# Kernel tuning notes

Measured on AMD Instinct MI355X. Metric: run time of the kernel, lower is better.

Reference implementation:

```python
import jax, jax.numpy as jnp
import numpy as np
import math

NUM_SEGS = 16  # label ids in gt are in [0, NUM_SEGS); 0 = background
NP_RATIO = 3
PI = np.float32(math.pi)


def cart2polar(coord):
    # coord: (N, 2, H, W) -> normalized polar angle in [0, 1)
    x = coord[:, 0]
    y = coord[:, 1]
    theta = jnp.arctan(y / (x + np.float32(1e-12)))
    theta = theta + (x < 0).astype(coord.dtype) * PI
    theta = theta + ((x > 0) & (y < 0)).astype(coord.dtype) * (2 * PI)
    return theta / (2 * PI)


def cal_weight(gt2d):
    # gt2d: (H, W) int labels. Per-segment average weight:
    # each pixel of segment s>0 gets (posCount / nSegPresent) / count(s).
    flat = gt2d.reshape(-1)
    counts = jnp.zeros((NUM_SEGS,), jnp.float32).at[flat].add(1.0)
    pos_counts = counts.at[0].set(0.0)  # labels = unique(gt)[1:] drops background 0
    pos_count = pos_counts.sum()
    nseg = (pos_counts > 0).sum().astype(jnp.float32)
    seg_ave = pos_count / jnp.maximum(nseg, 1.0)
    pix = seg_ave / jnp.maximum(counts, 1.0)  # per-label pixel weight
    return jnp.where(gt2d > 0, pix[gt2d], np.float32(0.0))


def setup_inputs() -> dict:
    key = jax.random.key(0)
    k1, k2, k3 = jax.random.split(key, 3)
    N, C, H, W = 8, 2, 1024, 1024
    pred = jax.random.normal(k1, (N, C, H, W), dtype=jnp.float32)
    gt_df = jax.random.normal(k2, (N, C, H, W), dtype=jnp.float32)
    gt = jax.random.randint(k3, (N, 1, H, W), 0, NUM_SEGS, dtype=jnp.int32)
    return {"pred": pred, "gt_df": gt_df, "gt": gt}


def reference(pred, gt_df, gt):
    N, _, H, W = pred.shape
    dist = pred - gt_df
    distL2 = dist * dist
    angle = cart2polar(gt_df) - cart2polar(pred)          # (N,H,W)
    term = distL2[:, 0] + distL2[:, 1] + angle * angle    # (N,H,W)

    weight = jax.vmap(lambda g: cal_weight(g[0]))(gt)     # (N,H,W) positive-region weights
    regionNeg = (weight == 0).astype(jnp.float32)
    sumPos = (weight > 0).astype(jnp.float32).sum(axis=(1, 2))
    sumNeg = regionNeg.sum(axis=(1, 2))
    k = jnp.minimum(NP_RATIO * sumPos, sumNeg).astype(jnp.int32)  # hard negatives per sample

    # OHEM: keep the k largest negative-region losses per sample
    lossFlat = (term * regionNeg).reshape(N, H * W)
    order = jnp.argsort(lossFlat, axis=1)
    rank = jnp.argsort(order, axis=1)  # rank of each element in ascending order
    keep = rank >= (H * W - k[:, None])
    mask = (keep & (lossFlat != 0)).astype(jnp.float32).reshape(N, H, W)  # weightNeg indicator

    # Faithful to torch broadcast: weightPos (N,H,W) + weightNeg (N,1,H,W) -> (N,N,H,W),
    # computed here without materializing the (N,N,H,W) tensor:
    # sum_{i,j,hw} term[j]*(weight[j] + mask[i]) = N*sum(term*weight) + sum_hw(term.sum(0)*mask.sum(0))
    num = N * jnp.sum(term * weight) + jnp.sum(term.sum(axis=0) * mask.sum(axis=0))
    denom = N * (weight.sum() + mask.sum())
    return num / N / 2.0 / denom
```

## Files before the change

kernel.cpp:

```cpp
#include <hip/hip_runtime.h>
#include <math.h>

#define NBATCH 8
#define HWN (1024*1024)
#define NGRP (HWN/4)
#define NSEG 16
#define N2B 512


static __device__ __forceinline__ float polar01(float x, float y) {
    float r = y * __builtin_amdgcn_rcpf(x + 1e-12f);
    float ar = fabsf(r);
    float inv = __builtin_amdgcn_rcpf(ar);
    bool big = ar > 1.0f;
    float t = big ? inv : ar;
    float s = t * t;
    float p = -0.0117212f;
    p = fmaf(p, s,  0.05265332f);
    p = fmaf(p, s, -0.11643287f);
    p = fmaf(p, s,  0.19354346f);
    p = fmaf(p, s, -0.33262348f);
    p = fmaf(p, s,  0.99997726f);
    float a = t * p;
    a = big ? (1.57079632679489662f - a) : a;
    a = copysignf(a, r);
    if (x < 0.f) a += 3.14159274101257324f;
    else if (x > 0.f && y < 0.f) a += 6.28318548202514648f;
    return a * 0.15915494309189535f;
}

static __device__ __forceinline__ void block_reduce2(double& a, double& b) {
    for (int o = 32; o; o >>= 1) { a += __shfl_down(a, o); b += __shfl_down(b, o); }
    __shared__ double sa[4], sb[4];
    int wave = threadIdx.x >> 6, lane = threadIdx.x & 63;
    if (lane == 0) { sa[wave] = a; sb[wave] = b; }
    __syncthreads();
    if (threadIdx.x == 0) {
        a = sa[0] + sa[1] + sa[2] + sa[3];
        b = sb[0] + sb[1] + sb[2] + sb[3];
    }
    __syncthreads();
}

__global__ __launch_bounds__(256) void k_fused(const float* __restrict__ pred,
        const float* __restrict__ gdf, const int* __restrict__ gt,
        float* __restrict__ lossBuf, unsigned short* __restrict__ tsumBuf,
        unsigned* __restrict__ h1G, unsigned* __restrict__ segCG,
        float* __restrict__ segSG) {
    __shared__ unsigned h1[NBATCH * 256];
    __shared__ unsigned sC[4][NBATCH * NSEG];
    __shared__ float    sS[4][NBATCH * NSEG];
    int tid = threadIdx.x, wave = tid >> 6;
    for (int i = tid; i < NBATCH * 256; i += 256) h1[i] = 0u;
    if (tid < NBATCH * NSEG) {
#pragma unroll
        for (int w = 0; w < 4; ++w) { sC[w][tid] = 0u; sS[w][tid] = 0.f; }
    }
    __syncthreads();

    int j = blockIdx.x * 256 + tid;
    float4 tsum = make_float4(0.f, 0.f, 0.f, 0.f);
#pragma unroll 2
    for (int n = 0; n < NBATCH; ++n) {
        float4 px4 = ((const float4*)(pred + ((size_t)(2 * n)    ) * HWN))[j];
        float4 py4 = ((const float4*)(pred + ((size_t)(2 * n) + 1) * HWN))[j];
        float4 gx4 = ((const float4*)(gdf  + ((size_t)(2 * n)    ) * HWN))[j];
        float4 gy4 = ((const float4*)(gdf  + ((size_t)(2 * n) + 1) * HWN))[j];
        int4   g4  = ((const int4*)  (gt   + (size_t)n * HWN))[j];
        float4 lossv;
#pragma unroll
        for (int e = 0; e < 4; ++e) {
            float px = (&px4.x)[e], py = (&py4.x)[e];
            float gx = (&gx4.x)[e], gy = (&gy4.x)[e];
            int   g  = (&g4.x)[e] & 15;
            float dx = px - gx, dy = py - gy;
            float ang = polar01(gx, gy) - polar01(px, py);
            float t = dx * dx + dy * dy + ang * ang;
            (&tsum.x)[e] += t;
            atomicAdd(&sC[wave][n * NSEG + g], 1u);
            atomicAdd(&sS[wave][n * NSEG + g], t);
            float lv = (g == 0) ? t : 0.f;
            (&lossv.x)[e] = lv;
            unsigned u = __float_as_uint(lv);
            if (u) atomicAdd(&h1[n * 256 + (u >> 24)], 1u);
        }
        ((float4*)(lossBuf + (size_t)n * HWN))[j] = lossv;
    }
    ushort4 tz;
#pragma unroll
    for (int e = 0; e < 4; ++e) {
        unsigned u = __float_as_uint((&tsum.x)[e]);
        (&tz.x)[e] = (unsigned short)((u + 0x7FFFu + ((u >> 16) & 1u)) >> 16);
    }
    ((ushort4*)tsumBuf)[j] = tz;

    __syncthreads();
    int copy = blockIdx.x & 31;
    if (tid < NBATCH * NSEG) {
        unsigned c = sC[0][tid] + sC[1][tid] + sC[2][tid] + sC[3][tid];
        float    s = sS[0][tid] + sS[1][tid] + sS[2][tid] + sS[3][tid];
        atomicAdd(&segCG[copy * (NBATCH * NSEG) + tid], c);
        atomicAdd(&segSG[copy * (NBATCH * NSEG) + tid], s);
    }
    for (int i = tid; i < NBATCH * 256; i += 256) {
        unsigned v = h1[i];
        if (v) atomicAdd(&h1G[copy * 2048 + i], v);
    }
}

__global__ void k_scanA(const unsigned* __restrict__ h1G, const unsigned* __restrict__ segCG,
                        const float* __restrict__ segSG, unsigned* __restrict__ stMode,
                        unsigned* __restrict__ stPfx, unsigned* __restrict__ stK,
                        unsigned* __restrict__ stT, double* __restrict__ num1w) {
    int n = blockIdx.x, tid = threadIdx.x;
    __shared__ unsigned h[256];
    __shared__ unsigned cc[NSEG];
    __shared__ double   sd[NSEG];
    unsigned hv = 0;
    for (int c = 0; c < 32; ++c) hv += h1G[c * 2048 + n * 256 + tid];
    h[tid] = hv;
    if (tid < NSEG) {
        unsigned cv = 0; double sv = 0.0;
        for (int c = 0; c < 32; ++c) {
            cv += segCG[c * (NBATCH * NSEG) + n * NSEG + tid];
            sv += (double)segSG[c * (NBATCH * NSEG) + n * NSEG + tid];
        }
        cc[tid] = cv; sd[tid] = sv;
    }
    __syncthreads();
    if (tid == 0) {
        long long sumPos = 0; int nseg = 0;
        for (int s = 1; s < NSEG; ++s) { sumPos += cc[s]; nseg += cc[s] ? 1 : 0; }
        long long sumNeg = cc[0];
        float seg_ave = (float)sumPos / (float)(nseg ? nseg : 1);
        double num1 = 0.0, wsum = 0.0;
        for (int s = 1; s < NSEG; ++s) {
            float pix = seg_ave / (float)(cc[s] ? cc[s] : 1u);
            num1 += (double)pix * sd[s];
            wsum += (double)pix * (double)cc[s];
        }
        num1w[2 * n] = num1; num1w[2 * n + 1] = wsum;
        long long k = 3 * sumPos; if (sumNeg < k) k = sumNeg;
        unsigned nnz = 0;
        for (int b = 0; b < 256; ++b) nnz += h[b];
        if (k <= 0)                      { stMode[n] = 0u; stT[n] = 0xFFFFFFFFu; stPfx[n] = 0u; stK[n] = 0u; }
        else if (k >= (long long)nnz)    { stMode[n] = 0u; stT[n] = 0u;          stPfx[n] = 0u; stK[n] = 0u; }
        else {
            unsigned cum = 0; int b1 = 0;
            for (int b = 255; b >= 0; --b) { if (cum + h[b] >= (unsigned)k) { b1 = b; break; } cum += h[b]; }
            stMode[n] = 1u; stPfx[n] = (unsigned)b1; stK[n] = (unsigned)k - cum; stT[n] = 0u;
        }
    }
}

__global__ __launch_bounds__(256) void k_refine(const float* __restrict__ lossBuf,
        const unsigned* __restrict__ stMode, const unsigned* __restrict__ stPfx,
        unsigned* __restrict__ hist, int level) {
    unsigned md[NBATCH], pf[NBATCH]; bool any = false;
#pragma unroll
    for (int n = 0; n < NBATCH; ++n) {
        md[n] = stMode[n]; pf[n] = stPfx[n];
        any = any || (md[n] == (unsigned)level);
    }
    if (!any) return;
    int ms = 32 - 8 * level, hs = 24 - 8 * level;
    int stride = gridDim.x * blockDim.x;
    for (int j = blockIdx.x * blockDim.x + threadIdx.x; j < NGRP; j += stride) {
#pragma unroll
        for (int n = 0; n < NBATCH; ++n) {
            if (md[n] != (unsigned)level) continue;
            float4 lv = ((const float4*)(lossBuf + (size_t)n * HWN))[j];
#pragma unroll
            for (int e = 0; e < 4; ++e) {
                unsigned u = __float_as_uint((&lv.x)[e]);
                if (u != 0u && (u >> ms) == pf[n])
                    atomicAdd(&hist[n * 256 + ((u >> hs) & 255u)], 1u);
            }
        }
    }
}

__global__ void k_scanN(unsigned* __restrict__ stMode, unsigned* __restrict__ stPfx,
                        unsigned* __restrict__ stK, unsigned* __restrict__ stT,
                        const unsigned* __restrict__ hist, int level) {
    int n = blockIdx.x;
    if (stMode[n] != (unsigned)level) return;
    __shared__ unsigned h[256];
    h[threadIdx.x] = hist[n * 256 + threadIdx.x];
    __syncthreads();
    if (threadIdx.x == 0) {
        unsigned k2 = stK[n], cum = 0; int bb = 0;
        for (int b = 255; b >= 0; --b) { if (cum + h[b] >= k2) { bb = b; break; } cum += h[b]; }
        unsigned np = (stPfx[n] << 8) | (unsigned)bb;
        stK[n] = k2 - cum;
        if (level == 3) { stT[n] = np; stMode[n] = 0u; }
        else            { stPfx[n] = np; stMode[n] = (unsigned)(level + 1); }
    }
}

__global__ __launch_bounds__(256) void k_num2(const float* __restrict__ lossBuf,
        const unsigned short* __restrict__ tsumBuf, const unsigned* __restrict__ stT,
        double* __restrict__ partB) {
    unsigned T[NBATCH];
#pragma unroll
    for (int n = 0; n < NBATCH; ++n) T[n] = stT[n];
    double acc = 0.0, cnt = 0.0;
    int stride = gridDim.x * blockDim.x;
    for (int j = blockIdx.x * blockDim.x + threadIdx.x; j < NGRP; j += stride) {
        ushort4 tz = ((const ushort4*)tsumBuf)[j];
        float ts[4];
#pragma unroll
        for (int e = 0; e < 4; ++e) ts[e] = __uint_as_float(((unsigned)(&tz.x)[e]) << 16);
#pragma unroll
        for (int n = 0; n < NBATCH; ++n) {
            float4 lv = ((const float4*)(lossBuf + (size_t)n * HWN))[j];
#pragma unroll
            for (int e = 0; e < 4; ++e) {
                unsigned u = __float_as_uint((&lv.x)[e]);
                if (u != 0u && u >= T[n]) { acc += (double)ts[e]; cnt += 1.0; }
            }
        }
    }
    block_reduce2(acc, cnt);
    if (threadIdx.x == 0) { partB[blockIdx.x * 2] = acc; partB[blockIdx.x * 2 + 1] = cnt; }
}

__global__ void k_result(const double* __restrict__ num1w, const double* __restrict__ partB,
                         float* __restrict__ out) {
    double c = 0.0, d = 0.0;
    for (int i = threadIdx.x; i < N2B; i += 256) { c += partB[2 * i]; d += partB[2 * i + 1]; }
    block_reduce2(c, d);
    if (threadIdx.x == 0) {
        double num1 = 0.0, wsum = 0.0;
        for (int n = 0; n < NBATCH; ++n) { num1 += num1w[2 * n]; wsum += num1w[2 * n + 1]; }
        double num = (double)NBATCH * num1 + c;
        double denom = (double)NBATCH * (wsum + d);
        out[0] = (float)(num / (double)NBATCH / 2.0 / denom);
    }
}


extern "C" void kernel_launch(void* const* d_in, const int* in_sizes, int n_in,
                              void* d_out, int out_size, void* d_ws, size_t ws_size,
                              hipStream_t stream) {
    const float* pred = (const float*)d_in[0];
    const float* gdf  = (const float*)d_in[1];
    const int*   gt   = (const int*)d_in[2];
    float* out = (float*)d_out;

    char* W = (char*)d_ws;
    float* lossBuf = (float*)W;
    unsigned short* tsumBuf = (unsigned short*)(W + 33554432);
    char* Z = W + 33554432 + 2097152;
    unsigned* h1G   = (unsigned*)Z;
    unsigned* segCG = (unsigned*)(Z + 262144);
    float*    segSG = (float*)  (Z + 262144 + 16384);
    unsigned* hA    = (unsigned*)(Z + 262144 + 32768);
    unsigned* hB    = hA + 2048;
    unsigned* hC    = hB + 2048;
    const size_t ZBYTES = 262144 + 32768 + 3 * 8192;
    char* P = Z + ZBYTES;
    unsigned* stMode = (unsigned*)P;
    unsigned* stPfx  = stMode + 8;
    unsigned* stK    = stMode + 16;
    unsigned* stT    = stMode + 24;
    double* num1w    = (double*)(P + 128);
    double* partB    = (double*)(P + 256);

    size_t need = 33554432 + 2097152 + ZBYTES + 256 + (size_t)N2B * 2 * 8;
    if (ws_size < need) return;

    hipMemsetAsync(Z, 0, ZBYTES, stream);
    k_fused <<<dim3(NGRP / 256), 256, 0, stream>>>(pred, gdf, gt, lossBuf, tsumBuf, h1G, segCG, segSG);
    k_scanA <<<NBATCH, 256, 0, stream>>>(h1G, segCG, segSG, stMode, stPfx, stK, stT, num1w);
    k_refine<<<256, 256, 0, stream>>>(lossBuf, stMode, stPfx, hA, 1);
    k_scanN <<<NBATCH, 256, 0, stream>>>(stMode, stPfx, stK, stT, hA, 1);
    k_refine<<<256, 256, 0, stream>>>(lossBuf, stMode, stPfx, hB, 2);
    k_scanN <<<NBATCH, 256, 0, stream>>>(stMode, stPfx, stK, stT, hB, 2);
    k_refine<<<256, 256, 0, stream>>>(lossBuf, stMode, stPfx, hC, 3);
    k_scanN <<<NBATCH, 256, 0, stream>>>(stMode, stPfx, stK, stT, hC, 3);
    k_num2  <<<N2B, 256, 0, stream>>>(lossBuf, tsumBuf, stT, partB);
    k_result<<<1, 256, 0, stream>>>(num1w, partB, out);
}
```

Measured before the change: 212.4 us.

## Precompute segment weights and skip OHEM selection when all negatives are kept

```diff
diff --git a/kernel.cpp b/kernel.cpp
--- a/kernel.cpp
+++ b/kernel.cpp
@@ -4,8 +4,7 @@
 #define NBATCH 8
 #define HWN (1024*1024)
 #define NGRP (HWN/4)
-#define NSEG 16
-#define N2B 512
+#define MAINB 1024
 
 
 static __device__ __forceinline__ float polar01(float x, float y) {
@@ -32,34 +31,111 @@
 static __device__ __forceinline__ void block_reduce2(double& a, double& b) {
     for (int o = 32; o; o >>= 1) { a += __shfl_down(a, o); b += __shfl_down(b, o); }
     __shared__ double sa[4], sb[4];
-    int wave = threadIdx.x >> 6, lane = threadIdx.x & 63;
-    if (lane == 0) { sa[wave] = a; sb[wave] = b; }
+    int w = threadIdx.x >> 6, l = threadIdx.x & 63;
+    if (l == 0) { sa[w] = a; sb[w] = b; }
+    __syncthreads();
+    if (threadIdx.x == 0) { a = sa[0]+sa[1]+sa[2]+sa[3]; b = sb[0]+sb[1]+sb[2]+sb[3]; }
+    __syncthreads();
+}
+
+static __device__ __forceinline__ void block_reduce3(double& a, double& b, double& c) {
+    for (int o = 32; o; o >>= 1) { a += __shfl_down(a, o); b += __shfl_down(b, o); c += __shfl_down(c, o); }
+    __shared__ double sa[4], sb[4], sc[4];
+    int w = threadIdx.x >> 6, l = threadIdx.x & 63;
+    if (l == 0) { sa[w] = a; sb[w] = b; sc[w] = c; }
     __syncthreads();
     if (threadIdx.x == 0) {
-        a = sa[0] + sa[1] + sa[2] + sa[3];
-        b = sb[0] + sb[1] + sb[2] + sb[3];
-    }
-    __syncthreads();
-}
-
-__global__ __launch_bounds__(256) void k_fused(const float* __restrict__ pred,
+        a = sa[0]+sa[1]+sa[2]+sa[3]; b = sb[0]+sb[1]+sb[2]+sb[3]; c = sc[0]+sc[1]+sc[2]+sc[3];
+    }
+    __syncthreads();
+}
+
+__global__ __launch_bounds__(256) void k_hist(const int* __restrict__ gt,
+        unsigned* __restrict__ countsRep) {
+    int tid = threadIdx.x;
+    int n = blockIdx.x >> 8;
+    int jb = blockIdx.x & 255;
+    const int4* g4 = (const int4*)(gt + (size_t)n * HWN);
+    unsigned c[16];
+#pragma unroll
+    for (int b = 0; b < 16; ++b) c[b] = 0u;
+#pragma unroll
+    for (int k = 0; k < 4; ++k) {
+        int4 g = g4[jb * 1024 + k * 256 + tid];
+#pragma unroll
+        for (int e = 0; e < 4; ++e) {
+            int gv = (&g.x)[e] & 15;
+#pragma unroll
+            for (int b = 0; b < 16; ++b) c[b] += (unsigned)__popcll(__ballot(gv == b));
+        }
+    }
+    if ((tid & 63) == 0) {
+        int copy = (blockIdx.x * 4 + (tid >> 6)) & 31;
+        unsigned* dst = countsRep + copy * 128 + n * 16;
+#pragma unroll
+        for (int b = 0; b < 16; ++b) atomicAdd(&dst[b], c[b]);
+    }
+}
+
+__global__ void k_stats(const unsigned* __restrict__ countsRep, float* __restrict__ pix,
+                        int* __restrict__ kv, int* __restrict__ mode,
+                        double* __restrict__ g_wsum, unsigned* __restrict__ anySlow) {
+    int tid = threadIdx.x;
+    __shared__ unsigned sc[128];
+    __shared__ int smd[NBATCH];
+    __shared__ double sws[NBATCH];
+    if (tid < 128) {
+        unsigned s = 0;
+        for (int c = 0; c < 32; ++c) s += countsRep[c * 128 + tid];
+        sc[tid] = s;
+    }
+    __syncthreads();
+    if (tid < NBATCH) {
+        int n = tid;
+        long long sumPos = 0; int nseg = 0;
+        for (int s = 1; s < 16; ++s) { sumPos += sc[n*16+s]; nseg += sc[n*16+s] ? 1 : 0; }
+        long long sumNeg = sc[n*16];
+        float seg_ave = (float)sumPos / (float)(nseg ? nseg : 1);
+        double ws = 0.0;
+        pix[n*16] = 0.f;
+        for (int s = 1; s < 16; ++s) {
+            unsigned cc = sc[n*16+s];
+            float pv = seg_ave / (float)(cc > 1u ? cc : 1u);
+            pix[n*16+s] = pv;
+            ws += (double)pv * (double)cc;
+        }
+        long long k = 3 * sumPos; if (sumNeg < k) k = sumNeg;
+        kv[n] = (int)k;
+        int md = (k <= 0) ? 0 : ((k >= sumNeg) ? 1 : 2);
+        mode[n] = md; smd[n] = md; sws[n] = ws;
+    }
+    __syncthreads();
+    if (tid == 0) {
+        double w = 0.0; unsigned as = 0u;
+        for (int i = 0; i < NBATCH; ++i) { w += sws[i]; as |= (smd[i] == 2) ? 1u : 0u; }
+        *g_wsum = w; *anySlow = as;
+    }
+}
+
+__global__ __launch_bounds__(256) void k_main(const float* __restrict__ pred,
         const float* __restrict__ gdf, const int* __restrict__ gt,
+        const float* __restrict__ pix, const int* __restrict__ mode,
         float* __restrict__ lossBuf, unsigned short* __restrict__ tsumBuf,
-        unsigned* __restrict__ h1G, unsigned* __restrict__ segCG,
-        float* __restrict__ segSG) {
+        unsigned* __restrict__ h1G, double* __restrict__ pN1,
+        double* __restrict__ pS2, double* __restrict__ pC) {
+    __shared__ float spix[128];
+    __shared__ int smode[NBATCH];
     __shared__ unsigned h1[NBATCH * 256];
-    __shared__ unsigned sC[4][NBATCH * NSEG];
-    __shared__ float    sS[4][NBATCH * NSEG];
-    int tid = threadIdx.x, wave = tid >> 6;
+    int tid = threadIdx.x;
+    if (tid < 128) spix[tid] = pix[tid];
+    if (tid < NBATCH) smode[tid] = mode[tid];
     for (int i = tid; i < NBATCH * 256; i += 256) h1[i] = 0u;
-    if (tid < NBATCH * NSEG) {
-#pragma unroll
-        for (int w = 0; w < 4; ++w) { sC[w][tid] = 0u; sS[w][tid] = 0.f; }
-    }
     __syncthreads();
 
     int j = blockIdx.x * 256 + tid;
-    float4 tsum = make_float4(0.f, 0.f, 0.f, 0.f);
+    float tsum[4] = {0.f, 0.f, 0.f, 0.f};
+    int   cntE[4] = {0, 0, 0, 0};
+    float num1f = 0.f;
 #pragma unroll 2
     for (int n = 0; n < NBATCH; ++n) {
         float4 px4 = ((const float4*)(pred + ((size_t)(2 * n)    ) * HWN))[j];
@@ -67,6 +143,7 @@
         float4 gx4 = ((const float4*)(gdf  + ((size_t)(2 * n)    ) * HWN))[j];
         float4 gy4 = ((const float4*)(gdf  + ((size_t)(2 * n) + 1) * HWN))[j];
         int4   g4  = ((const int4*)  (gt   + (size_t)n * HWN))[j];
+        int m = smode[n];
         float4 lossv;
 #pragma unroll
         for (int e = 0; e < 4; ++e) {
@@ -76,93 +153,88 @@
             float dx = px - gx, dy = py - gy;
             float ang = polar01(gx, gy) - polar01(px, py);
             float t = dx * dx + dy * dy + ang * ang;
-            (&tsum.x)[e] += t;
-            atomicAdd(&sC[wave][n * NSEG + g], 1u);
-            atomicAdd(&sS[wave][n * NSEG + g], t);
-            float lv = (g == 0) ? t : 0.f;
-            (&lossv.x)[e] = lv;
-            unsigned u = __float_as_uint(lv);
-            if (u) atomicAdd(&h1[n * 256 + (u >> 24)], 1u);
-        }
-        ((float4*)(lossBuf + (size_t)n * HWN))[j] = lossv;
+            tsum[e] += t;
+            num1f += t * spix[n * 16 + g];
+            if (m == 1) {
+                if (g == 0 && t != 0.f) cntE[e]++;
+            } else if (m == 2) {
+                float lv = (g == 0) ? t : 0.f;
+                (&lossv.x)[e] = lv;
+                unsigned u = __float_as_uint(lv);
+                if (u) atomicAdd(&h1[n * 256 + (u >> 24)], 1u);
+            }
+        }
+        if (m == 2) ((float4*)(lossBuf + (size_t)n * HWN))[j] = lossv;
     }
     ushort4 tz;
 #pragma unroll
     for (int e = 0; e < 4; ++e) {
-        unsigned u = __float_as_uint((&tsum.x)[e]);
+        unsigned u = __float_as_uint(tsum[e]);
         (&tz.x)[e] = (unsigned short)((u + 0x7FFFu + ((u >> 16) & 1u)) >> 16);
     }
     ((ushort4*)tsumBuf)[j] = tz;
 
-    __syncthreads();
-    int copy = blockIdx.x & 31;
-    if (tid < NBATCH * NSEG) {
-        unsigned c = sC[0][tid] + sC[1][tid] + sC[2][tid] + sC[3][tid];
-        float    s = sS[0][tid] + sS[1][tid] + sS[2][tid] + sS[3][tid];
-        atomicAdd(&segCG[copy * (NBATCH * NSEG) + tid], c);
-        atomicAdd(&segSG[copy * (NBATCH * NSEG) + tid], s);
-    }
+    float spec2 = 0.f, cntS = 0.f;
+#pragma unroll
+    for (int e = 0; e < 4; ++e) { spec2 += tsum[e] * (float)cntE[e]; cntS += (float)cntE[e]; }
+
+    double a = (double)num1f, b = (double)spec2, c = (double)cntS;
+    block_reduce3(a, b, c);
+    if (tid == 0) { pN1[blockIdx.x] = a; pS2[blockIdx.x] = b; pC[blockIdx.x] = c; }
+
+    __syncthreads();
+    int copy = blockIdx.x & 7;
     for (int i = tid; i < NBATCH * 256; i += 256) {
         unsigned v = h1[i];
         if (v) atomicAdd(&h1G[copy * 2048 + i], v);
     }
 }
 
-__global__ void k_scanA(const unsigned* __restrict__ h1G, const unsigned* __restrict__ segCG,
-                        const float* __restrict__ segSG, unsigned* __restrict__ stMode,
-                        unsigned* __restrict__ stPfx, unsigned* __restrict__ stK,
-                        unsigned* __restrict__ stT, double* __restrict__ num1w) {
-    int n = blockIdx.x, tid = threadIdx.x;
+__global__ void k_scanA(const unsigned* __restrict__ h1G, const int* __restrict__ kv,
+        const int* __restrict__ mode, unsigned* __restrict__ stMode,
+        unsigned* __restrict__ stPfx, unsigned* __restrict__ stK,
+        unsigned* __restrict__ stT, unsigned* __restrict__ active,
+        const double* __restrict__ pN1, const double* __restrict__ pS2,
+        const double* __restrict__ pC, double* __restrict__ g_num1,
+        double* __restrict__ g_acc, double* __restrict__ g_cnt) {
+    int tid = threadIdx.x;
+    double a = 0, b = 0, c = 0;
+    for (int i = tid; i < MAINB; i += 256) { a += pN1[i]; b += pS2[i]; c += pC[i]; }
+    block_reduce3(a, b, c);
+    if (tid == 0) { *g_num1 = a; *g_acc = b; *g_cnt = c; }
     __shared__ unsigned h[256];
-    __shared__ unsigned cc[NSEG];
-    __shared__ double   sd[NSEG];
-    unsigned hv = 0;
-    for (int c = 0; c < 32; ++c) hv += h1G[c * 2048 + n * 256 + tid];
-    h[tid] = hv;
-    if (tid < NSEG) {
-        unsigned cv = 0; double sv = 0.0;
-        for (int c = 0; c < 32; ++c) {
-            cv += segCG[c * (NBATCH * NSEG) + n * NSEG + tid];
-            sv += (double)segSG[c * (NBATCH * NSEG) + n * NSEG + tid];
-        }
-        cc[tid] = cv; sd[tid] = sv;
-    }
-    __syncthreads();
-    if (tid == 0) {
-        long long sumPos = 0; int nseg = 0;
-        for (int s = 1; s < NSEG; ++s) { sumPos += cc[s]; nseg += cc[s] ? 1 : 0; }
-        long long sumNeg = cc[0];
-        float seg_ave = (float)sumPos / (float)(nseg ? nseg : 1);
-        double num1 = 0.0, wsum = 0.0;
-        for (int s = 1; s < NSEG; ++s) {
-            float pix = seg_ave / (float)(cc[s] ? cc[s] : 1u);
-            num1 += (double)pix * sd[s];
-            wsum += (double)pix * (double)cc[s];
-        }
-        num1w[2 * n] = num1; num1w[2 * n + 1] = wsum;
-        long long k = 3 * sumPos; if (sumNeg < k) k = sumNeg;
-        unsigned nnz = 0;
-        for (int b = 0; b < 256; ++b) nnz += h[b];
-        if (k <= 0)                      { stMode[n] = 0u; stT[n] = 0xFFFFFFFFu; stPfx[n] = 0u; stK[n] = 0u; }
-        else if (k >= (long long)nnz)    { stMode[n] = 0u; stT[n] = 0u;          stPfx[n] = 0u; stK[n] = 0u; }
-        else {
-            unsigned cum = 0; int b1 = 0;
-            for (int b = 255; b >= 0; --b) { if (cum + h[b] >= (unsigned)k) { b1 = b; break; } cum += h[b]; }
-            stMode[n] = 1u; stPfx[n] = (unsigned)b1; stK[n] = (unsigned)k - cum; stT[n] = 0u;
-        }
+    __shared__ unsigned rw[4];
+    for (int n = 0; n < NBATCH; ++n) {
+        if (mode[n] != 2) continue;
+        unsigned s = 0;
+        for (int c8 = 0; c8 < 8; ++c8) s += h1G[c8 * 2048 + n * 256 + tid];
+        h[tid] = s;
+        unsigned v = s;
+        for (int o = 32; o; o >>= 1) v += __shfl_down(v, o);
+        int w = tid >> 6, l = tid & 63;
+        if (l == 0) rw[w] = v;
+        __syncthreads();
+        if (tid == 0) {
+            unsigned nnz = rw[0] + rw[1] + rw[2] + rw[3];
+            unsigned k = (unsigned)kv[n];
+            if (k >= nnz) { stT[n] = 0u; stMode[n] = 0u; }
+            else {
+                unsigned cum = 0; int b1 = 0;
+                for (int bb = 255; bb >= 0; --bb) { if (cum + h[bb] >= k) { b1 = bb; break; } cum += h[bb]; }
+                stMode[n] = 1u; stPfx[n] = (unsigned)b1; stK[n] = k - cum; active[1] = 1u;
+            }
+        }
+        __syncthreads();
     }
 }
 
 __global__ __launch_bounds__(256) void k_refine(const float* __restrict__ lossBuf,
         const unsigned* __restrict__ stMode, const unsigned* __restrict__ stPfx,
-        unsigned* __restrict__ hist, int level) {
-    unsigned md[NBATCH], pf[NBATCH]; bool any = false;
-#pragma unroll
-    for (int n = 0; n < NBATCH; ++n) {
-        md[n] = stMode[n]; pf[n] = stPfx[n];
-        any = any || (md[n] == (unsigned)level);
-    }
-    if (!any) return;
+        unsigned* __restrict__ hist, int level, const unsigned* __restrict__ active) {
+    if (active[level] == 0u) return;
+    unsigned md[NBATCH], pf[NBATCH];
+#pragma unroll
+    for (int n = 0; n < NBATCH; ++n) { md[n] = stMode[n]; pf[n] = stPfx[n]; }
     int ms = 32 - 8 * level, hs = 24 - 8 * level;
     int stride = gridDim.x * blockDim.x;
     for (int j = blockIdx.x * blockDim.x + threadIdx.x; j < NGRP; j += stride) {
@@ -181,8 +253,9 @@
 }
 
 __global__ void k_scanN(unsigned* __restrict__ stMode, unsigned* __restrict__ stPfx,
-                        unsigned* __restrict__ stK, unsigned* __restrict__ stT,
-                        const unsigned* __restrict__ hist, int level) {
+        unsigned* __restrict__ stK, unsigned* __restrict__ stT,
+        const unsigned* __restrict__ hist, int level, unsigned* __restrict__ active) {
+    if (active[level] == 0u) return;
     int n = blockIdx.x;
     if (stMode[n] != (unsigned)level) return;
     __shared__ unsigned h[256];
@@ -194,49 +267,42 @@
         unsigned np = (stPfx[n] << 8) | (unsigned)bb;
         stK[n] = k2 - cum;
         if (level == 3) { stT[n] = np; stMode[n] = 0u; }
-        else            { stPfx[n] = np; stMode[n] = (unsigned)(level + 1); }
+        else            { stPfx[n] = np; stMode[n] = (unsigned)(level + 1); active[level + 1] = 1u; }
     }
 }
 
 __global__ __launch_bounds__(256) void k_num2(const float* __restrict__ lossBuf,
         const unsigned short* __restrict__ tsumBuf, const unsigned* __restrict__ stT,
-        double* __restrict__ partB) {
-    unsigned T[NBATCH];
-#pragma unroll
-    for (int n = 0; n < NBATCH; ++n) T[n] = stT[n];
+        const int* __restrict__ mode, const unsigned* __restrict__ anySlow,
+        double* __restrict__ g_acc, double* __restrict__ g_cnt) {
+    if (*anySlow == 0u) return;
+    int j = blockIdx.x * 256 + threadIdx.x;
+    ushort4 tz = ((const ushort4*)tsumBuf)[j];
+    float ts[4];
+#pragma unroll
+    for (int e = 0; e < 4; ++e) ts[e] = __uint_as_float(((unsigned)(&tz.x)[e]) << 16);
     double acc = 0.0, cnt = 0.0;
-    int stride = gridDim.x * blockDim.x;
-    for (int j = blockIdx.x * blockDim.x + threadIdx.x; j < NGRP; j += stride) {
-        ushort4 tz = ((const ushort4*)tsumBuf)[j];
-        float ts[4];
-#pragma unroll
-        for (int e = 0; e < 4; ++e) ts[e] = __uint_as_float(((unsigned)(&tz.x)[e]) << 16);
-#pragma unroll
-        for (int n = 0; n < NBATCH; ++n) {
-            float4 lv = ((const float4*)(lossBuf + (size_t)n * HWN))[j];
-#pragma unroll
-            for (int e = 0; e < 4; ++e) {
-                unsigned u = __float_as_uint((&lv.x)[e]);
-                if (u != 0u && u >= T[n]) { acc += (double)ts[e]; cnt += 1.0; }
-            }
+#pragma unroll
+    for (int n = 0; n < NBATCH; ++n) {
+        if (mode[n] != 2) continue;
+        unsigned T = stT[n];
+        float4 lv = ((const float4*)(lossBuf + (size_t)n * HWN))[j];
+#pragma unroll
+        for (int e = 0; e < 4; ++e) {
+            unsigned u = __float_as_uint((&lv.x)[e]);
+            if (u != 0u && u >= T) { acc += (double)ts[e]; cnt += 1.0; }
         }
     }
     block_reduce2(acc, cnt);
-    if (threadIdx.x == 0) { partB[blockIdx.x * 2] = acc; partB[blockIdx.x * 2 + 1] = cnt; }
-}
-
-__global__ void k_result(const double* __restrict__ num1w, const double* __restrict__ partB,
-                         float* __restrict__ out) {
-    double c = 0.0, d = 0.0;
-    for (int i = threadIdx.x; i < N2B; i += 256) { c += partB[2 * i]; d += partB[2 * i + 1]; }
-    block_reduce2(c, d);
-    if (threadIdx.x == 0) {
-        double num1 = 0.0, wsum = 0.0;
-        for (int n = 0; n < NBATCH; ++n) { num1 += num1w[2 * n]; wsum += num1w[2 * n + 1]; }
-        double num = (double)NBATCH * num1 + c;
-        double denom = (double)NBATCH * (wsum + d);
-        out[0] = (float)(num / (double)NBATCH / 2.0 / denom);
-    }
+    if (threadIdx.x == 0) { atomicAdd(g_acc, acc); atomicAdd(g_cnt, cnt); }
+}
+
+__global__ void k_result(const double* __restrict__ g_num1, const double* __restrict__ g_wsum,
+        const double* __restrict__ g_acc, const double* __restrict__ g_cnt,
+        float* __restrict__ out) {
+    double num = (double)NBATCH * g_num1[0] + g_acc[0];
+    double den = (double)NBATCH * (g_wsum[0] + g_cnt[0]);
+    out[0] = (float)(num / (double)NBATCH / 2.0 / den);
 }
 
 
@@ -251,34 +317,47 @@
     char* W = (char*)d_ws;
     float* lossBuf = (float*)W;
     unsigned short* tsumBuf = (unsigned short*)(W + 33554432);
-    char* Z = W + 33554432 + 2097152;
-    unsigned* h1G   = (unsigned*)Z;
-    unsigned* segCG = (unsigned*)(Z + 262144);
-    float*    segSG = (float*)  (Z + 262144 + 16384);
-    unsigned* hA    = (unsigned*)(Z + 262144 + 32768);
-    unsigned* hB    = hA + 2048;
-    unsigned* hC    = hB + 2048;
-    const size_t ZBYTES = 262144 + 32768 + 3 * 8192;
+    char* Z = W + 35651584;
+    unsigned* countsRep = (unsigned*)Z;
+    unsigned* h1G    = (unsigned*)(Z + 16384);
+    unsigned* hA     = (unsigned*)(Z + 81920);
+    unsigned* hB     = (unsigned*)(Z + 90112);
+    unsigned* hC     = (unsigned*)(Z + 98304);
+    unsigned* stMode = (unsigned*)(Z + 106496);
+    unsigned* stPfx  = (unsigned*)(Z + 106528);
+    unsigned* stK    = (unsigned*)(Z + 106560);
+    unsigned* stT    = (unsigned*)(Z + 106592);
+    unsigned* active = (unsigned*)(Z + 106624);
+    unsigned* anySlow= (unsigned*)(Z + 106640);
+    double*   g_num1 = (double*)(Z + 106648);
+    double*   g_wsum = (double*)(Z + 106656);
+    double*   g_acc  = (double*)(Z + 106664);
+    double*   g_cnt  = (double*)(Z + 106672);
+    const size_t ZBYTES = 106680;
     char* P = Z + ZBYTES;
-    unsigned* stMode = (unsigned*)P;
-    unsigned* stPfx  = stMode + 8;
-    unsigned* stK    = stMode + 16;
-    unsigned* stT    = stMode + 24;
-    double* num1w    = (double*)(P + 128);
-    double* partB    = (double*)(P + 256);
-
-    size_t need = 33554432 + 2097152 + ZBYTES + 256 + (size_t)N2B * 2 * 8;
+    float* pix  = (float*)P;
+    int*   kv   = (int*)(P + 512);
+    int*   mode = (int*)(P + 544);
+    double* pN1 = (double*)(P + 576);
+    double* pS2 = (double*)(P + 8768);
+    double* pC  = (double*)(P + 16960);
+
+    size_t need = 35651584 + ZBYTES + 25152;
     if (ws_size < need) return;
 
     hipMemsetAsync(Z, 0, ZBYTES, stream);
-    k_fused <<<dim3(NGRP / 256), 256, 0, stream>>>(pred, gdf, gt, lossBuf, tsumBuf, h1G, segCG, segSG);
-    k_scanA <<<NBATCH, 256, 0, stream>>>(h1G, segCG, segSG, stMode, stPfx, stK, stT, num1w);
-    k_refine<<<256, 256, 0, stream>>>(lossBuf, stMode, stPfx, hA, 1);
-    k_scanN <<<NBATCH, 256, 0, stream>>>(stMode, stPfx, stK, stT, hA, 1);
-    k_refine<<<256, 256, 0, stream>>>(lossBuf, stMode, stPfx, hB, 2);
-    k_scanN <<<NBATCH, 256, 0, stream>>>(stMode, stPfx, stK, stT, hB, 2);
-    k_refine<<<256, 256, 0, stream>>>(lossBuf, stMode, stPfx, hC, 3);
-    k_scanN <<<NBATCH, 256, 0, stream>>>(stMode, stPfx, stK, stT, hC, 3);
-    k_num2  <<<N2B, 256, 0, stream>>>(lossBuf, tsumBuf, stT, partB);
-    k_result<<<1, 256, 0, stream>>>(num1w, partB, out);
-}
+    k_hist  <<<2048, 256, 0, stream>>>(gt, countsRep);
+    k_stats <<<1, 256, 0, stream>>>(countsRep, pix, kv, mode, g_wsum, anySlow);
+    k_main  <<<MAINB, 256, 0, stream>>>(pred, gdf, gt, pix, mode, lossBuf, tsumBuf,
+                                        h1G, pN1, pS2, pC);
+    k_scanA <<<1, 256, 0, stream>>>(h1G, kv, mode, stMode, stPfx, stK, stT, active,
+                                    pN1, pS2, pC, g_num1, g_acc, g_cnt);
+    k_refine<<<1024, 256, 0, stream>>>(lossBuf, stMode, stPfx, hA, 1, active);
+    k_scanN <<<NBATCH, 256, 0, stream>>>(stMode, stPfx, stK, stT, hA, 1, active);
+    k_refine<<<1024, 256, 0, stream>>>(lossBuf, stMode, stPfx, hB, 2, active);
+    k_scanN <<<NBATCH, 256, 0, stream>>>(stMode, stPfx, stK, stT, hB, 2, active);
+    k_refine<<<1024, 256, 0, stream>>>(lossBuf, stMode, stPfx, hC, 3, active);
+    k_scanN <<<NBATCH, 256, 0, stream>>>(stMode, stPfx, stK, stT, hC, 3, active);
+    k_num2  <<<MAINB, 256, 0, stream>>>(lossBuf, tsumBuf, stT, mode, anySlow, g_acc, g_cnt);
+    k_result<<<1, 1, 0, stream>>>(g_num1, g_wsum, g_acc, g_cnt, out);
+}
```

Result: slower. 223.1 us (+5.1%).
